# Kernel optimization log

Measured on AMD Instinct MI355X. Metric: run time of the kernel, lower is better.

Reference implementation:

```python
import jax, jax.numpy as jnp
import numpy as np

V, E, H, B, S, O, L = 50257, 256, 512, 64, 1024, 1, 2


def setup_inputs() -> dict:
    key = jax.random.key(0)
    ks = jax.random.split(key, 16)
    s = 0.02
    d = {
        "tokens": jax.random.randint(ks[0], (B, S), 0, V),
        "emb": jax.random.normal(ks[1], (V, E), jnp.float32) * s,
        "fc_w": jax.random.normal(ks[2], (O, H), jnp.float32) * s,
        "fc_b": jnp.zeros((O,), jnp.float32),
    }
    ins = [E, H]
    for l in range(L):
        i = ins[l]
        d[f"gate_w{l}"] = jax.random.normal(ks[3 + 4 * l], (2 * H, i + H), jnp.float32) * s
        d[f"gate_b{l}"] = jnp.zeros((2 * H,), jnp.float32)
        d[f"gi_w{l}"] = jax.random.normal(ks[4 + 4 * l], (H, i), jnp.float32) * s
        d[f"gi_b{l}"] = jnp.zeros((H,), jnp.float32)
        d[f"gh_w{l}"] = jax.random.normal(ks[5 + 4 * l], (H, H), jnp.float32) * s
        d[f"gh_b{l}"] = jnp.zeros((H,), jnp.float32)
    return d


def _cell(x, h, gw, gb, giw, gib, ghw, ghb):
    # gates from concat(input, hidden): [B, 2H]
    gates = jnp.concatenate([x, h], axis=-1) @ gw.T + gb
    r, z = jnp.split(gates, 2, axis=-1)
    r = jax.nn.sigmoid(r)
    z = jax.nn.sigmoid(z)
    n = jnp.tanh(x @ giw.T + gib + r * (h @ ghw.T + ghb))
    return (1.0 - z) * n + z * h  # dropout is identity at inference


def _forward(tokens, emb, fc_w, fc_b, layers):
    x = emb[tokens]  # [B, S, E]
    b = tokens.shape[0]
    h0 = tuple(jnp.zeros((b, H), x.dtype) for _ in layers)

    def step(hs, xt):  # xt: [B, E]
        new = []
        inp = xt
        for h, p in zip(hs, layers):
            h = _cell(inp, h, *p)
            new.append(h)
            inp = h
        return tuple(new), None

    hs, _ = jax.lax.scan(step, h0, jnp.swapaxes(x, 0, 1))  # scan over S
    out = hs[-1] @ fc_w.T + fc_b  # [B, 1]
    return jax.nn.sigmoid(jnp.squeeze(out))  # [B]


def reference(tokens, emb, fc_w, fc_b,
              gate_w0, gate_b0, gi_w0, gi_b0, gh_w0, gh_b0,
              gate_w1, gate_b1, gi_w1, gi_b1, gh_w1, gh_b1):
    layers = [
        (gate_w0, gate_b0, gi_w0, gi_b0, gh_w0, gh_b0),
        (gate_w1, gate_b1, gi_w1, gi_b1, gh_w1, gh_b1),
    ]
    return _forward(tokens, emb, fc_w, fc_b, layers)
```

## Files before the change

### kernel.cpp

```cpp
#include <hip/hip_runtime.h>

typedef _Float16 f16;
typedef _Float16 f16x8 __attribute__((ext_vector_type(8)));
typedef float f32x4 __attribute__((ext_vector_type(4)));
typedef unsigned long long u64;

#define B_ 64
#define S_ 1024
#define E_ 256
#define H_ 512
#define NG 1536
#define TCH 128
#define NCHUNK (S_/TCH)
#define ROWS_CH (TCH*B_)
#define HS_LD 544

__device__ __forceinline__ float sigm(float x) { return 1.f / (1.f + __expf(-x)); }

#define ALOAD(p) __hip_atomic_load((p), __ATOMIC_RELAXED, __HIP_MEMORY_SCOPE_AGENT)
#define ASTORE(p, v) __hip_atomic_store((p), (v), __ATOMIC_RELAXED, __HIP_MEMORY_SCOPE_AGENT)

__global__ __launch_bounds__(256) void k_embed(const int* __restrict__ tok,
        const float* __restrict__ emb, f16* __restrict__ X, int t0) {
    int idx = blockIdx.x * 256 + threadIdx.x;
    int r = idx >> 6;
    int c4 = (idx & 63) << 2;
    int t = t0 + (r >> 6), b = r & 63;
    int tk = tok[b * S_ + t];
    float4 v = *reinterpret_cast<const float4*>(emb + (size_t)tk * E_ + c4);
    union { f16 h[4]; u64 u; } w;
    w.h[0] = (f16)v.x; w.h[1] = (f16)v.y; w.h[2] = (f16)v.z; w.h[3] = (f16)v.w;
    *reinterpret_cast<u64*>(X + (size_t)r * E_ + c4) = w.u;
}

__global__ __launch_bounds__(256) void k_packW(const float* __restrict__ gw, int ld, int off,
        const float* __restrict__ g2, f16* __restrict__ W, int KK) {
    int idx = blockIdx.x * 256 + threadIdx.x;
    int per = KK >> 2;
    if (idx >= NG * per) return;
    int row = idx / per;
    int c4 = (idx % per) << 2;
    const float* src = (row < 1024) ? gw + (size_t)row * ld + off + c4
                                    : g2 + (size_t)(row - 1024) * KK + c4;
    float4 v = *reinterpret_cast<const float4*>(src);
    union { f16 h[4]; u64 u; } w;
    w.h[0] = (f16)v.x; w.h[1] = (f16)v.y; w.h[2] = (f16)v.z; w.h[3] = (f16)v.w;
    *reinterpret_cast<u64*>(W + (size_t)row * KK + c4) = w.u;
}

__global__ __launch_bounds__(256) void k_packBias(const float* __restrict__ gb,
        const float* __restrict__ gib, float* __restrict__ bias) {
    int i = blockIdx.x * 256 + threadIdx.x;
    if (i < 1024) bias[i] = gb[i];
    else if (i < NG) bias[i] = gib[i - 1024];
}

__global__ __launch_bounds__(256) void k_gemm(const f16* __restrict__ A,
        const f16* __restrict__ Bm, const float* __restrict__ bias,
        f16* __restrict__ C, int K) {
    __shared__ f16 As[64][40];
    __shared__ f16 Bs[64][40];
    const int tid = threadIdx.x;
    const int m0 = blockIdx.y << 6, n0 = blockIdx.x << 6;
    const int w = tid >> 6, l = tid & 63;
    const int wr = (w >> 1) << 5, wc = (w & 1) << 5;
    const int srow = tid >> 2, sc8 = (tid & 3) << 3;
    const int fr = l & 15, kl = (l >> 4) << 3;
    f32x4 acc[2][2] = {};
    for (int k0 = 0; k0 < K; k0 += 32) {
        *reinterpret_cast<f16x8*>(&As[srow][sc8]) =
            *reinterpret_cast<const f16x8*>(A + (size_t)(m0 + srow) * K + k0 + sc8);
        *reinterpret_cast<f16x8*>(&Bs[srow][sc8]) =
            *reinterpret_cast<const f16x8*>(Bm + (size_t)(n0 + srow) * K + k0 + sc8);
        __syncthreads();
        f16x8 a0 = *reinterpret_cast<const f16x8*>(&As[wr + fr][kl]);
        f16x8 a1 = *reinterpret_cast<const f16x8*>(&As[wr + 16 + fr][kl]);
        f16x8 b0 = *reinterpret_cast<const f16x8*>(&Bs[wc + fr][kl]);
        f16x8 b1 = *reinterpret_cast<const f16x8*>(&Bs[wc + 16 + fr][kl]);
        acc[0][0] = __builtin_amdgcn_mfma_f32_16x16x32_f16(a0, b0, acc[0][0], 0, 0, 0);
        acc[0][1] = __builtin_amdgcn_mfma_f32_16x16x32_f16(a0, b1, acc[0][1], 0, 0, 0);
        acc[1][0] = __builtin_amdgcn_mfma_f32_16x16x32_f16(a1, b0, acc[1][0], 0, 0, 0);
        acc[1][1] = __builtin_amdgcn_mfma_f32_16x16x32_f16(a1, b1, acc[1][1], 0, 0, 0);
        __syncthreads();
    }
    for (int fm = 0; fm < 2; ++fm)
        for (int fn = 0; fn < 2; ++fn) {
            int col = n0 + wc + (fn << 4) + fr;
            float bv = bias[col];
            for (int j = 0; j < 4; ++j) {
                int rowg = m0 + wr + (fm << 4) + ((l >> 4) << 2) + j;
                C[(size_t)rowg * NG + col] = (f16)(acc[fm][fn][j] + bv);
            }
        }
}

__global__ __launch_bounds__(256, 1) void k_recur4(
        const f16* __restrict__ Wh0p, const f16* __restrict__ Wh1p,
        const f16* __restrict__ Z0, const f16* __restrict__ Z1,
        const float* __restrict__ ghb0, const float* __restrict__ ghb1,
        u64* ring0, u64* ring1, f16* __restrict__ H0out, f16* __restrict__ h1out,
        int t00, int n0, int t01, int n1) {
    __shared__ __align__(16) f16 HS[8][HS_LD];
    __shared__ __align__(16) f16 hx[8][40];
    const int blk = blockIdx.x;
    const int c = blk & 7;
    const int l = (blk >> 3) & 1;
    const int gg = blk >> 4;
    const int nsteps = l ? n1 : n0;
    if (nsteps <= 0) return;
    const int t0 = l ? t01 : t00;
    const f16* __restrict__ Wh = l ? Wh1p : Wh0p;
    const f16* __restrict__ Z  = l ? Z1 : Z0;
    const float* __restrict__ ghb = l ? ghb1 : ghb0;
    u64* ring = l ? ring1 : ring0;

    const int i0 = gg << 5;
    const int tid = threadIdx.x;
    const int w = tid >> 6;
    const int lane = tid & 63;
    const int colb = lane & 15;
    const int bq = lane & 7;
    const int j4 = lane >> 4;
    const int rrow = lane & 15;
    const int ol = rrow >> 2, gate = rrow & 3;

    f16x8 wA[2][16];
    #pragma unroll
    for (int tl = 0; tl < 2; ++tl) {
        const int out = i0 + (w << 3) + (tl << 2) + ol;
        #pragma unroll
        for (int t = 0; t < 16; ++t) {
            f16x8 v{};
            if (gate < 3)
                v = *reinterpret_cast<const f16x8*>(
                        Wh + ((size_t)(gate * H_ + out)) * H_ + (t << 5) + (j4 << 3));
            wA[tl][t] = v;
        }
    }
    const int outA = i0 + (w << 3) + j4;
    const int outB = outA + 4;
    const float gbA = ghb[outA], gbB = ghb[outB];

    for (int sl = 0; sl < nsteps; ++sl) {
        const int s = t0 + sl;
        const size_t zrow = ((size_t)sl * 64 + (c << 3) + bq) * NG;
        float zrA = (float)Z[zrow + outA];
        float zzA = (float)Z[zrow + H_ + outA];
        float znA = (float)Z[zrow + 2 * H_ + outA];
        float zrB = (float)Z[zrow + outB];
        float zzB = (float)Z[zrow + H_ + outB];
        float znB = (float)Z[zrow + 2 * H_ + outB];
        {
            const u64* src = ring + ((size_t)(s & 3) * 8 + c) * 2048;
            u64 g[8];
            #pragma unroll
            for (int i = 0; i < 8; ++i) g[i] = ALOAD(src + (i << 8) + tid);
            #pragma unroll
            for (int i = 0; i < 8; ++i) {
                while ((unsigned)(g[i] >> 32) != (unsigned)s)
                    g[i] = ALOAD(src + (i << 8) + tid);
                *reinterpret_cast<unsigned*>(
                    &HS[i][((tid >> 4) << 5) + ((tid & 15) << 1)]) = (unsigned)g[i];
            }
        }
        __syncthreads();
        f32x4 a00{}, a01{}, a10{}, a11{};
        #pragma unroll
        for (int t = 0; t < 16; ++t) {
            f16x8 bf = *reinterpret_cast<const f16x8*>(&HS[bq][(t << 5) + (j4 << 3)]);
            if (t & 1) {
                a01 = __builtin_amdgcn_mfma_f32_16x16x32_f16(wA[0][t], bf, a01, 0, 0, 0);
                a11 = __builtin_amdgcn_mfma_f32_16x16x32_f16(wA[1][t], bf, a11, 0, 0, 0);
            } else {
                a00 = __builtin_amdgcn_mfma_f32_16x16x32_f16(wA[0][t], bf, a00, 0, 0, 0);
                a10 = __builtin_amdgcn_mfma_f32_16x16x32_f16(wA[1][t], bf, a10, 0, 0, 0);
            }
        }
        f32x4 dA = a00 + a01;
        f32x4 dB = a10 + a11;
        if (colb < 8) {
            float holdA = (float)HS[bq][outA];
            float holdB = (float)HS[bq][outB];
            float rA = sigm(zrA + dA[0]);
            float zA = sigm(zzA + dA[1]);
            float nA = tanhf(znA + rA * (dA[2] + gbA));
            float rB = sigm(zrB + dB[0]);
            float zB = sigm(zzB + dB[1]);
            float nB = tanhf(znB + rB * (dB[2] + gbB));
            hx[bq][(w << 3) + j4]     = (f16)((1.f - zA) * nA + zA * holdA);
            hx[bq][(w << 3) + 4 + j4] = (f16)((1.f - zB) * nB + zB * holdB);
        }
        __syncthreads();
        if (tid < 128) {
            const int b = tid >> 4, d = tid & 15;
            unsigned dval = *reinterpret_cast<const unsigned*>(&hx[b][d << 1]);
            u64 gr = ((u64)(unsigned)(s + 1) << 32) | (u64)dval;
            ASTORE(ring + ((size_t)((s + 1) & 3) * 8 + c) * 2048
                        + ((size_t)b << 8) + (gg << 4) + d, gr);
            if (l == 0)
                *reinterpret_cast<unsigned*>(
                    &H0out[((size_t)sl * 64 + (c << 3) + b) * H_ + i0 + (d << 1)]) = dval;
            else if (s == S_ - 1)
                *reinterpret_cast<unsigned*>(
                    &h1out[((size_t)(c << 3) + b) * H_ + i0 + (d << 1)]) = dval;
        }
        __syncthreads();
    }
}

__global__ __launch_bounds__(64) void k_final(const f16* __restrict__ h,
        const float* __restrict__ fcw, const float* __restrict__ fcb,
        float* __restrict__ out) {
    int b = threadIdx.x;
    float acc = fcb[0];
    for (int k = 0; k < H_; ++k) acc += (float)h[(size_t)b * H_ + k] * fcw[k];
    out[b] = sigm(acc);
}

extern "C" void kernel_launch(void* const* d_in, const int* in_sizes, int n_in,
                              void* d_out, int out_size, void* d_ws, size_t ws_size,
                              hipStream_t stream) {
    (void)in_sizes; (void)n_in; (void)out_size; (void)ws_size;
    const int*   tokens = (const int*)d_in[0];
    const float* emb  = (const float*)d_in[1];
    const float* fc_w = (const float*)d_in[2];
    const float* fc_b = (const float*)d_in[3];
    const float* gw0  = (const float*)d_in[4];
    const float* gb0  = (const float*)d_in[5];
    const float* giw0 = (const float*)d_in[6];
    const float* gib0 = (const float*)d_in[7];
    const float* ghw0 = (const float*)d_in[8];
    const float* ghb0 = (const float*)d_in[9];
    const float* gw1  = (const float*)d_in[10];
    const float* gb1  = (const float*)d_in[11];
    const float* giw1 = (const float*)d_in[12];
    const float* gib1 = (const float*)d_in[13];
    const float* ghw1 = (const float*)d_in[14];
    const float* ghb1 = (const float*)d_in[15];

    char* base = (char*)d_ws;
    size_t off = 0;
    auto carve = [&](size_t bytes) {
        char* p = base + off;
        off = (off + bytes + 255) & ~(size_t)255;
        return p;
    };
    f16*   Wx0   = (f16*)carve((size_t)NG * 256 * 2);
    f16*   Wh0   = (f16*)carve((size_t)NG * 512 * 2);
    f16*   Wx1   = (f16*)carve((size_t)NG * 512 * 2);
    f16*   Wh1   = (f16*)carve((size_t)NG * 512 * 2);
    float* bias0 = (float*)carve(NG * 4);
    float* bias1 = (float*)carve(NG * 4);
    u64*   ring0 = (u64*)carve((size_t)4 * 8 * 2048 * 8);
    u64*   ring1 = (u64*)carve((size_t)4 * 8 * 2048 * 8);
    f16*   h1out = (f16*)carve((size_t)B_ * H_ * 2);
    f16*   Xc    = (f16*)carve((size_t)ROWS_CH * 256 * 2);
    f16*   Zc0   = (f16*)carve((size_t)ROWS_CH * NG * 2);
    f16*   H0c   = (f16*)carve((size_t)ROWS_CH * 512 * 2);
    f16*   Zc1   = (f16*)carve((size_t)ROWS_CH * NG * 2);

    hipMemsetAsync(ring0, 0, (size_t)4 * 8 * 2048 * 8, stream);
    hipMemsetAsync(ring1, 0, (size_t)4 * 8 * 2048 * 8, stream);

    k_packW<<<384, 256, 0, stream>>>(gw0, 768, 0,    giw0, Wx0, 256);
    k_packW<<<768, 256, 0, stream>>>(gw0, 768, 256,  ghw0, Wh0, 512);
    k_packW<<<768, 256, 0, stream>>>(gw1, 1024, 0,   giw1, Wx1, 512);
    k_packW<<<768, 256, 0, stream>>>(gw1, 1024, 512, ghw1, Wh1, 512);
    k_packBias<<<6, 256, 0, stream>>>(gb0, gib0, bias0);
    k_packBias<<<6, 256, 0, stream>>>(gb1, gib1, bias1);

    dim3 gemmGrid(NG / 64, ROWS_CH / 64);
    for (int ch = 0; ch < NCHUNK; ++ch) {
        int t0 = ch * TCH;
        k_embed<<<ROWS_CH * 64 / 256, 256, 0, stream>>>(tokens, emb, Xc, t0);
        k_gemm<<<gemmGrid, 256, 0, stream>>>(Xc, Wx0, bias0, Zc0, 256);
        k_recur4<<<256, 256, 0, stream>>>(Wh0, Wh1, Zc0, Zc1, ghb0, ghb1,
                                          ring0, ring1, H0c, h1out,
                                          t0, TCH, t0 - TCH, ch ? TCH : 0);
        k_gemm<<<gemmGrid, 256, 0, stream>>>(H0c, Wx1, bias1, Zc1, 512);
    }
    k_recur4<<<256, 256, 0, stream>>>(Wh0, Wh1, Zc0, Zc1, ghb0, ghb1,
                                      ring0, ring1, H0c, h1out,
                                      0, 0, (NCHUNK - 1) * TCH, TCH);
    k_final<<<1, 64, 0, stream>>>(h1out, fc_w, fc_b, (float*)d_out);
}
```

Before: 3.143 ms.

## Double-buffer recurrent hidden state, publish directly from lanes, prefetch next Z

After: 5.002 ms. 1.59x slower.

```diff
diff --git a/kernel.cpp b/kernel.cpp
--- a/kernel.cpp
+++ b/kernel.cpp
@@ -94,14 +94,13 @@
         }
 }
 
-__global__ __launch_bounds__(256, 1) void k_recur4(
+__global__ __launch_bounds__(256, 1) void k_recur5(
         const f16* __restrict__ Wh0p, const f16* __restrict__ Wh1p,
         const f16* __restrict__ Z0, const f16* __restrict__ Z1,
         const float* __restrict__ ghb0, const float* __restrict__ ghb1,
         u64* ring0, u64* ring1, f16* __restrict__ H0out, f16* __restrict__ h1out,
         int t00, int n0, int t01, int n1) {
-    __shared__ __align__(16) f16 HS[8][HS_LD];
-    __shared__ __align__(16) f16 hx[8][40];
+    __shared__ __align__(16) f16 HS[2][8][HS_LD];
     const int blk = blockIdx.x;
     const int c = blk & 7;
     const int l = (blk >> 3) & 1;
@@ -141,33 +140,61 @@
     const int outB = outA + 4;
     const float gbA = ghb[outA], gbB = ghb[outB];
 
+    float zrA, zzA, znA, zrB, zzB, znB;
+    {
+        const size_t zrow = ((size_t)(c << 3) + bq) * NG;
+        zrA = (float)Z[zrow + outA]; zzA = (float)Z[zrow + H_ + outA];
+        znA = (float)Z[zrow + 2 * H_ + outA];
+        zrB = (float)Z[zrow + outB]; zzB = (float)Z[zrow + H_ + outB];
+        znB = (float)Z[zrow + 2 * H_ + outB];
+    }
+
     for (int sl = 0; sl < nsteps; ++sl) {
         const int s = t0 + sl;
-        const size_t zrow = ((size_t)sl * 64 + (c << 3) + bq) * NG;
-        float zrA = (float)Z[zrow + outA];
-        float zzA = (float)Z[zrow + H_ + outA];
-        float znA = (float)Z[zrow + 2 * H_ + outA];
-        float zrB = (float)Z[zrow + outB];
-        float zzB = (float)Z[zrow + H_ + outB];
-        float znB = (float)Z[zrow + 2 * H_ + outB];
+        f16* Hc = &HS[sl & 1][0][0];
         {
             const u64* src = ring + ((size_t)(s & 3) * 8 + c) * 2048;
             u64 g[8];
             #pragma unroll
             for (int i = 0; i < 8; ++i) g[i] = ALOAD(src + (i << 8) + tid);
+            unsigned miss = 0;
             #pragma unroll
             for (int i = 0; i < 8; ++i) {
-                while ((unsigned)(g[i] >> 32) != (unsigned)s)
-                    g[i] = ALOAD(src + (i << 8) + tid);
-                *reinterpret_cast<unsigned*>(
-                    &HS[i][((tid >> 4) << 5) + ((tid & 15) << 1)]) = (unsigned)g[i];
+                if ((unsigned)(g[i] >> 32) == (unsigned)s) {
+                    const int rest = tid, b = i;
+                    const int og = ((rest >> 4) << 5) + (((rest >> 2) & 3) << 3) + (rest & 3);
+                    Hc[b * HS_LD + og]     = __builtin_bit_cast(f16, (unsigned short)(g[i] & 0xffff));
+                    Hc[b * HS_LD + og + 4] = __builtin_bit_cast(f16, (unsigned short)((g[i] >> 16) & 0xffff));
+                } else miss |= 1u << i;
+            }
+            while (miss) {
+                #pragma unroll
+                for (int i = 0; i < 8; ++i)
+                    if (miss & (1u << i)) g[i] = ALOAD(src + (i << 8) + tid);
+                #pragma unroll
+                for (int i = 0; i < 8; ++i)
+                    if ((miss & (1u << i)) && (unsigned)(g[i] >> 32) == (unsigned)s) {
+                        const int rest = tid, b = i;
+                        const int og = ((rest >> 4) << 5) + (((rest >> 2) & 3) << 3) + (rest & 3);
+                        Hc[b * HS_LD + og]     = __builtin_bit_cast(f16, (unsigned short)(g[i] & 0xffff));
+                        Hc[b * HS_LD + og + 4] = __builtin_bit_cast(f16, (unsigned short)((g[i] >> 16) & 0xffff));
+                        miss &= ~(1u << i);
+                    }
             }
         }
         __syncthreads();
+        float nrA = 0, nzA = 0, nnA = 0, nrB = 0, nzB = 0, nnB = 0;
+        if (sl + 1 < nsteps) {
+            const size_t zrow = ((size_t)(sl + 1) * 64 + (c << 3) + bq) * NG;
+            nrA = (float)Z[zrow + outA]; nzA = (float)Z[zrow + H_ + outA];
+            nnA = (float)Z[zrow + 2 * H_ + outA];
+            nrB = (float)Z[zrow + outB]; nzB = (float)Z[zrow + H_ + outB];
+            nnB = (float)Z[zrow + 2 * H_ + outB];
+        }
         f32x4 a00{}, a01{}, a10{}, a11{};
         #pragma unroll
         for (int t = 0; t < 16; ++t) {
-            f16x8 bf = *reinterpret_cast<const f16x8*>(&HS[bq][(t << 5) + (j4 << 3)]);
+            f16x8 bf = *reinterpret_cast<const f16x8*>(&Hc[bq * HS_LD + (t << 5) + (j4 << 3)]);
             if (t & 1) {
                 a01 = __builtin_amdgcn_mfma_f32_16x16x32_f16(wA[0][t], bf, a01, 0, 0, 0);
                 a11 = __builtin_amdgcn_mfma_f32_16x16x32_f16(wA[1][t], bf, a11, 0, 0, 0);
@@ -179,32 +206,30 @@
         f32x4 dA = a00 + a01;
         f32x4 dB = a10 + a11;
         if (colb < 8) {
-            float holdA = (float)HS[bq][outA];
-            float holdB = (float)HS[bq][outB];
+            float holdA = (float)Hc[bq * HS_LD + outA];
+            float holdB = (float)Hc[bq * HS_LD + outB];
             float rA = sigm(zrA + dA[0]);
             float zA = sigm(zzA + dA[1]);
             float nA = tanhf(znA + rA * (dA[2] + gbA));
             float rB = sigm(zrB + dB[0]);
             float zB = sigm(zzB + dB[1]);
             float nB = tanhf(znB + rB * (dB[2] + gbB));
-            hx[bq][(w << 3) + j4]     = (f16)((1.f - zA) * nA + zA * holdA);
-            hx[bq][(w << 3) + 4 + j4] = (f16)((1.f - zB) * nB + zB * holdB);
-        }
-        __syncthreads();
-        if (tid < 128) {
-            const int b = tid >> 4, d = tid & 15;
-            unsigned dval = *reinterpret_cast<const unsigned*>(&hx[b][d << 1]);
-            u64 gr = ((u64)(unsigned)(s + 1) << 32) | (u64)dval;
-            ASTORE(ring + ((size_t)((s + 1) & 3) * 8 + c) * 2048
-                        + ((size_t)b << 8) + (gg << 4) + d, gr);
-            if (l == 0)
-                *reinterpret_cast<unsigned*>(
-                    &H0out[((size_t)sl * 64 + (c << 3) + b) * H_ + i0 + (d << 1)]) = dval;
-            else if (s == S_ - 1)
-                *reinterpret_cast<unsigned*>(
-                    &h1out[((size_t)(c << 3) + b) * H_ + i0 + (d << 1)]) = dval;
-        }
-        __syncthreads();
+            f16 hA = (f16)((1.f - zA) * nA + zA * holdA);
+            f16 hB = (f16)((1.f - zB) * nB + zB * holdB);
+            unsigned short uA = __builtin_bit_cast(unsigned short, hA);
+            unsigned short uB = __builtin_bit_cast(unsigned short, hB);
+            u64 gr = ((u64)(unsigned)(s + 1) << 32) | ((u64)uB << 16) | (u64)uA;
+            const size_t gi = ((size_t)bq << 8) + (gg << 4) + (w << 2) + j4;
+            ASTORE(ring + ((size_t)((s + 1) & 3) * 8 + c) * 2048 + gi, gr);
+            if (l == 0) {
+                f16* hp = H0out + ((size_t)sl * 64 + (c << 3) + bq) * H_;
+                hp[outA] = hA; hp[outB] = hB;
+            } else if (s == S_ - 1) {
+                f16* hp = h1out + ((size_t)(c << 3) + bq) * H_;
+                hp[outA] = hA; hp[outB] = hB;
+            }
+        }
+        zrA = nrA; zzA = nzA; znA = nnA; zrB = nrB; zzB = nzB; znB = nnB;
     }
 }
 
@@ -274,12 +299,12 @@
         int t0 = ch * TCH;
         k_embed<<<ROWS_CH * 64 / 256, 256, 0, stream>>>(tokens, emb, Xc, t0);
         k_gemm<<<gemmGrid, 256, 0, stream>>>(Xc, Wx0, bias0, Zc0, 256);
-        k_recur4<<<256, 256, 0, stream>>>(Wh0, Wh1, Zc0, Zc1, ghb0, ghb1,
+        k_recur5<<<256, 256, 0, stream>>>(Wh0, Wh1, Zc0, Zc1, ghb0, ghb1,
                                           ring0, ring1, H0c, h1out,
                                           t0, TCH, t0 - TCH, ch ? TCH : 0);
         k_gemm<<<gemmGrid, 256, 0, stream>>>(H0c, Wx1, bias1, Zc1, 512);
     }
-    k_recur4<<<256, 256, 0, stream>>>(Wh0, Wh1, Zc0, Zc1, ghb0, ghb1,
+    k_recur5<<<256, 256, 0, stream>>>(Wh0, Wh1, Zc0, Zc1, ghb0, ghb1,
                                       ring0, ring1, H0c, h1out,
                                       0, 0, (NCHUNK - 1) * TCH, TCH);
     k_final<<<1, 64, 0, stream>>>(h1out, fc_w, fc_b, (float*)d_out);
```

## Fuse chunked GEMMs and recurrence into one persistent producer-consumer megakernel

Applied to the files above, without the earlier changes.

After: 3.568 ms. 1.14x slower.

```diff
diff --git a/kernel.cpp b/kernel.cpp
--- a/kernel.cpp
+++ b/kernel.cpp
@@ -10,27 +10,25 @@
 #define E_ 256
 #define H_ 512
 #define NG 1536
-#define TCH 128
-#define NCHUNK (S_/TCH)
-#define ROWS_CH (TCH*B_)
+#define V_ 50257
 #define HS_LD 544
+#define ZSLOT 32
+#define DSLOT 64
 
 __device__ __forceinline__ float sigm(float x) { return 1.f / (1.f + __expf(-x)); }
 
 #define ALOAD(p) __hip_atomic_load((p), __ATOMIC_RELAXED, __HIP_MEMORY_SCOPE_AGENT)
 #define ASTORE(p, v) __hip_atomic_store((p), (v), __ATOMIC_RELAXED, __HIP_MEMORY_SCOPE_AGENT)
-
-__global__ __launch_bounds__(256) void k_embed(const int* __restrict__ tok,
-        const float* __restrict__ emb, f16* __restrict__ X, int t0) {
-    int idx = blockIdx.x * 256 + threadIdx.x;
-    int r = idx >> 6;
-    int c4 = (idx & 63) << 2;
-    int t = t0 + (r >> 6), b = r & 63;
-    int tk = tok[b * S_ + t];
-    float4 v = *reinterpret_cast<const float4*>(emb + (size_t)tk * E_ + c4);
-    union { f16 h[4]; u64 u; } w;
-    w.h[0] = (f16)v.x; w.h[1] = (f16)v.y; w.h[2] = (f16)v.z; w.h[3] = (f16)v.w;
-    *reinterpret_cast<u64*>(X + (size_t)r * E_ + c4) = w.u;
+#define AADD(p, v) __hip_atomic_fetch_add((p), (v), __ATOMIC_RELAXED, __HIP_MEMORY_SCOPE_AGENT)
+
+__device__ __forceinline__ float zxt(u64 g, int odd) {
+    unsigned short u = (unsigned short)(odd ? (g >> 16) : g);
+    return (float)__builtin_bit_cast(f16, u);
+}
+__device__ __forceinline__ u64 pk2(float a, float b) {
+    unsigned short ua = __builtin_bit_cast(unsigned short, (f16)a);
+    unsigned short ub = __builtin_bit_cast(unsigned short, (f16)b);
+    return (u64)ua | ((u64)ub << 16);
 }
 
 __global__ __launch_bounds__(256) void k_packW(const float* __restrict__ gw, int ld, int off,
@@ -55,156 +53,279 @@
     else if (i < NG) bias[i] = gib[i - 1024];
 }
 
-__global__ __launch_bounds__(256) void k_gemm(const f16* __restrict__ A,
-        const f16* __restrict__ Bm, const float* __restrict__ bias,
-        f16* __restrict__ C, int K) {
-    __shared__ f16 As[64][40];
-    __shared__ f16 Bs[64][40];
+__global__ __launch_bounds__(256) void k_embconv(const float* __restrict__ emb,
+        f16* __restrict__ out) {
+    long long i = (long long)blockIdx.x * 256 + threadIdx.x;
+    if (i >= (long long)V_ * E_ / 4) return;
+    float4 v = reinterpret_cast<const float4*>(emb)[i];
+    union { f16 h[4]; u64 u; } w;
+    w.h[0] = (f16)v.x; w.h[1] = (f16)v.y; w.h[2] = (f16)v.z; w.h[3] = (f16)v.w;
+    reinterpret_cast<u64*>(out)[i] = w.u;
+}
+
+__global__ __launch_bounds__(256, 2) void k_mega(
+    const f16* __restrict__ Wx0, const f16* __restrict__ Wh0,
+    const f16* __restrict__ Wx1, const f16* __restrict__ Wh1,
+    const float* __restrict__ bias0c, const float* __restrict__ bias1c,
+    const float* __restrict__ ghb0, const float* __restrict__ ghb1,
+    const int* __restrict__ tok, const f16* __restrict__ embh,
+    u64* ring0, u64* ring1, u64* d0r, u64* z0r, u64* z1r,
+    int* zflag1, f16* __restrict__ h1out)
+{
+    __shared__ __align__(16) unsigned char LDS_[65536];
+    const int blk = blockIdx.x;
     const int tid = threadIdx.x;
-    const int m0 = blockIdx.y << 6, n0 = blockIdx.x << 6;
-    const int w = tid >> 6, l = tid & 63;
-    const int wr = (w >> 1) << 5, wc = (w & 1) << 5;
-    const int srow = tid >> 2, sc8 = (tid & 3) << 3;
-    const int fr = l & 15, kl = (l >> 4) << 3;
-    f32x4 acc[2][2] = {};
-    for (int k0 = 0; k0 < K; k0 += 32) {
-        *reinterpret_cast<f16x8*>(&As[srow][sc8]) =
-            *reinterpret_cast<const f16x8*>(A + (size_t)(m0 + srow) * K + k0 + sc8);
-        *reinterpret_cast<f16x8*>(&Bs[srow][sc8]) =
-            *reinterpret_cast<const f16x8*>(Bm + (size_t)(n0 + srow) * K + k0 + sc8);
-        __syncthreads();
-        f16x8 a0 = *reinterpret_cast<const f16x8*>(&As[wr + fr][kl]);
-        f16x8 a1 = *reinterpret_cast<const f16x8*>(&As[wr + 16 + fr][kl]);
-        f16x8 b0 = *reinterpret_cast<const f16x8*>(&Bs[wc + fr][kl]);
-        f16x8 b1 = *reinterpret_cast<const f16x8*>(&Bs[wc + 16 + fr][kl]);
-        acc[0][0] = __builtin_amdgcn_mfma_f32_16x16x32_f16(a0, b0, acc[0][0], 0, 0, 0);
-        acc[0][1] = __builtin_amdgcn_mfma_f32_16x16x32_f16(a0, b1, acc[0][1], 0, 0, 0);
-        acc[1][0] = __builtin_amdgcn_mfma_f32_16x16x32_f16(a1, b0, acc[1][0], 0, 0, 0);
-        acc[1][1] = __builtin_amdgcn_mfma_f32_16x16x32_f16(a1, b1, acc[1][1], 0, 0, 0);
-        __syncthreads();
-    }
-    for (int fm = 0; fm < 2; ++fm)
-        for (int fn = 0; fn < 2; ++fn) {
-            int col = n0 + wc + (fn << 4) + fr;
-            float bv = bias[col];
-            for (int j = 0; j < 4; ++j) {
-                int rowg = m0 + wr + (fm << 4) + ((l >> 4) << 2) + j;
-                C[(size_t)rowg * NG + col] = (f16)(acc[fm][fn][j] + bv);
+
+    if (blk < 256) {
+        const int l = blk >> 7;
+        const int q = blk & 127;
+        const int c = q & 7, gg = q >> 3;
+        const int i0 = gg << 5;
+        const int w = tid >> 6, lane = tid & 63;
+        const int colb = lane & 15, bq = lane & 7, j4 = lane >> 4;
+        const int rrow = lane & 15;
+        const int ol = rrow >> 2, gate = rrow & 3;
+        const f16* Wh = l ? Wh1 : Wh0;
+        const float* ghb = l ? ghb1 : ghb0;
+        u64* ring = l ? ring1 : ring0;
+        const u64* zr = l ? z1r : z0r;
+        f16* HS = (f16*)LDS_;
+        f16* hx = (f16*)(LDS_ + 8 * HS_LD * 2);
+
+        f16x8 wA[2][16];
+        #pragma unroll
+        for (int tl = 0; tl < 2; ++tl) {
+            const int out = i0 + (w << 3) + (tl << 2) + ol;
+            #pragma unroll
+            for (int t = 0; t < 16; ++t) {
+                f16x8 v{};
+                if (gate < 3)
+                    v = *reinterpret_cast<const f16x8*>(
+                            Wh + ((size_t)(gate * H_ + out)) * H_ + (t << 5) + (j4 << 3));
+                wA[tl][t] = v;
             }
         }
-}
-
-__global__ __launch_bounds__(256, 1) void k_recur4(
-        const f16* __restrict__ Wh0p, const f16* __restrict__ Wh1p,
-        const f16* __restrict__ Z0, const f16* __restrict__ Z1,
-        const float* __restrict__ ghb0, const float* __restrict__ ghb1,
-        u64* ring0, u64* ring1, f16* __restrict__ H0out, f16* __restrict__ h1out,
-        int t00, int n0, int t01, int n1) {
-    __shared__ __align__(16) f16 HS[8][HS_LD];
-    __shared__ __align__(16) f16 hx[8][40];
-    const int blk = blockIdx.x;
-    const int c = blk & 7;
-    const int l = (blk >> 3) & 1;
-    const int gg = blk >> 4;
-    const int nsteps = l ? n1 : n0;
-    if (nsteps <= 0) return;
-    const int t0 = l ? t01 : t00;
-    const f16* __restrict__ Wh = l ? Wh1p : Wh0p;
-    const f16* __restrict__ Z  = l ? Z1 : Z0;
-    const float* __restrict__ ghb = l ? ghb1 : ghb0;
-    u64* ring = l ? ring1 : ring0;
-
-    const int i0 = gg << 5;
-    const int tid = threadIdx.x;
-    const int w = tid >> 6;
-    const int lane = tid & 63;
-    const int colb = lane & 15;
-    const int bq = lane & 7;
-    const int j4 = lane >> 4;
-    const int rrow = lane & 15;
-    const int ol = rrow >> 2, gate = rrow & 3;
-
-    f16x8 wA[2][16];
-    #pragma unroll
-    for (int tl = 0; tl < 2; ++tl) {
-        const int out = i0 + (w << 3) + (tl << 2) + ol;
+        const int outA = i0 + (w << 3) + j4, outB = outA + 4;
+        const float gbA = ghb[outA], gbB = ghb[outB];
+        const int batch = (c << 3) + bq;
+        const int par = j4 & 1;
+        const size_t zoA = (size_t)(outA >> 1), zoB = (size_t)(outB >> 1);
+
+        for (int s = 0; s < S_; ++s) {
+            const u64* zs = zr + (size_t)(s & (ZSLOT - 1)) * 49152 + (size_t)batch * 768;
+            u64 zg0 = ALOAD(zs + zoA),        zg1 = ALOAD(zs + zoB);
+            u64 zg2 = ALOAD(zs + 256 + zoA),  zg3 = ALOAD(zs + 256 + zoB);
+            u64 zg4 = ALOAD(zs + 512 + zoA),  zg5 = ALOAD(zs + 512 + zoB);
+            if (!l && s >= 64) {
+                const int* zf = zflag1 + (s - 60);
+                while (ALOAD(zf) < 24) {}
+            }
+            {
+                const u64* src = ring + ((size_t)(s & 3) * 8 + c) * 2048;
+                u64 g[8];
+                #pragma unroll
+                for (int i = 0; i < 8; ++i) g[i] = ALOAD(src + (i << 8) + tid);
+                #pragma unroll
+                for (int i = 0; i < 8; ++i) {
+                    while ((unsigned)(g[i] >> 32) != (unsigned)s)
+                        g[i] = ALOAD(src + (i << 8) + tid);
+                    *reinterpret_cast<unsigned*>(
+                        &HS[i * HS_LD + ((tid >> 4) << 5) + ((tid & 15) << 1)]) = (unsigned)g[i];
+                }
+            }
+            const unsigned ztg = (unsigned)(s + 1);
+            while ((unsigned)(zg0 >> 32) != ztg) zg0 = ALOAD(zs + zoA);
+            while ((unsigned)(zg1 >> 32) != ztg) zg1 = ALOAD(zs + zoB);
+            while ((unsigned)(zg2 >> 32) != ztg) zg2 = ALOAD(zs + 256 + zoA);
+            while ((unsigned)(zg3 >> 32) != ztg) zg3 = ALOAD(zs + 256 + zoB);
+            while ((unsigned)(zg4 >> 32) != ztg) zg4 = ALOAD(zs + 512 + zoA);
+            while ((unsigned)(zg5 >> 32) != ztg) zg5 = ALOAD(zs + 512 + zoB);
+            __syncthreads();
+            f32x4 a00{}, a01{}, a10{}, a11{};
+            #pragma unroll
+            for (int t = 0; t < 16; ++t) {
+                f16x8 bf = *reinterpret_cast<const f16x8*>(&HS[bq * HS_LD + (t << 5) + (j4 << 3)]);
+                if (t & 1) {
+                    a01 = __builtin_amdgcn_mfma_f32_16x16x32_f16(wA[0][t], bf, a01, 0, 0, 0);
+                    a11 = __builtin_amdgcn_mfma_f32_16x16x32_f16(wA[1][t], bf, a11, 0, 0, 0);
+                } else {
+                    a00 = __builtin_amdgcn_mfma_f32_16x16x32_f16(wA[0][t], bf, a00, 0, 0, 0);
+                    a10 = __builtin_amdgcn_mfma_f32_16x16x32_f16(wA[1][t], bf, a10, 0, 0, 0);
+                }
+            }
+            f32x4 dA = a00 + a01, dB = a10 + a11;
+            if (colb < 8) {
+                float holdA = (float)HS[bq * HS_LD + outA];
+                float holdB = (float)HS[bq * HS_LD + outB];
+                float rA = sigm(zxt(zg0, par) + dA[0]);
+                float zA = sigm(zxt(zg2, par) + dA[1]);
+                float nA = tanhf(zxt(zg4, par) + rA * (dA[2] + gbA));
+                float rB = sigm(zxt(zg1, par) + dB[0]);
+                float zB = sigm(zxt(zg3, par) + dB[1]);
+                float nB = tanhf(zxt(zg5, par) + rB * (dB[2] + gbB));
+                hx[bq * 40 + (w << 3) + j4]     = (f16)((1.f - zA) * nA + zA * holdA);
+                hx[bq * 40 + (w << 3) + 4 + j4] = (f16)((1.f - zB) * nB + zB * holdB);
+            }
+            __syncthreads();
+            if (tid < 128) {
+                const int b = tid >> 4, d = tid & 15;
+                unsigned dval = *reinterpret_cast<const unsigned*>(&hx[b * 40 + (d << 1)]);
+                u64 gr = ((u64)(unsigned)(s + 1) << 32) | (u64)dval;
+                const size_t gi = ((size_t)b << 8) + (gg << 4) + d;
+                ASTORE(ring + ((size_t)((s + 1) & 3) * 8 + c) * 2048 + gi, gr);
+                if (!l)
+                    ASTORE(d0r + ((size_t)((s + 1) & (DSLOT - 1)) * 8 + c) * 2048 + gi, gr);
+                else if (s == S_ - 1)
+                    *reinterpret_cast<unsigned*>(
+                        &h1out[((size_t)(c << 3) + b) * H_ + i0 + (d << 1)]) = dval;
+            }
+            __syncthreads();
+        }
+    } else if (blk < 352) {
+        const int qq = blk - 256, p = qq & 3, nt = qq >> 2;
+        const int n0 = nt << 6;
+        const int w = tid >> 6, lane = tid & 63;
+        const int q4 = lane >> 4, l15 = lane & 15;
+        f16* hst = (f16*)LDS_;
+        f16x8 wxa[16];
+        const int arow = n0 + (w << 4) + l15;
         #pragma unroll
-        for (int t = 0; t < 16; ++t) {
-            f16x8 v{};
-            if (gate < 3)
-                v = *reinterpret_cast<const f16x8*>(
-                        Wh + ((size_t)(gate * H_ + out)) * H_ + (t << 5) + (j4 << 3));
-            wA[tl][t] = v;
+        for (int t = 0; t < 16; ++t)
+            wxa[t] = *reinterpret_cast<const f16x8*>(Wx1 + (size_t)arow * 512 + (t << 5) + (q4 << 3));
+        const int cb = n0 + (w << 4) + (q4 << 2);
+        const float bv0 = bias1c[cb], bv1 = bias1c[cb + 1], bv2 = bias1c[cb + 2], bv3 = bias1c[cb + 3];
+        const int sx = (l15 & 7) << 3;
+
+        for (int t = p; t < S_; t += 4) {
+            if (t >= 32) {
+                const u64* pr = ring1 + ((size_t)((t - 28) & 3) * 8 + (lane & 7)) * 2048;
+                while (!__all((int)(unsigned)(ALOAD(pr) >> 32) >= t - 28)) {}
+            }
+            {
+                const u64* src = d0r + (size_t)((t + 1) & (DSLOT - 1)) * 16384;
+                const unsigned tg = (unsigned)(t + 1);
+                #pragma unroll
+                for (int hf = 0; hf < 4; ++hf) {
+                    u64 g[16]; unsigned miss = 0;
+                    #pragma unroll
+                    for (int j = 0; j < 16; ++j) g[j] = ALOAD(src + (hf << 12) + (j << 8) + tid);
+                    #pragma unroll
+                    for (int j = 0; j < 16; ++j) {
+                        int idx = (hf << 12) + (j << 8) + tid;
+                        int bt = idx >> 8, col = (idx & 255) << 1;
+                        if ((unsigned)(g[j] >> 32) == tg)
+                            *reinterpret_cast<unsigned*>(&hst[bt * 512 + (col ^ ((bt & 7) << 3))]) = (unsigned)g[j];
+                        else miss |= 1u << j;
+                    }
+                    while (miss) {
+                        #pragma unroll
+                        for (int j = 0; j < 16; ++j) if (miss & (1u << j)) {
+                            u64 v = ALOAD(src + (hf << 12) + (j << 8) + tid);
+                            if ((unsigned)(v >> 32) == tg) {
+                                int idx = (hf << 12) + (j << 8) + tid;
+                                int bt = idx >> 8, col = (idx & 255) << 1;
+                                *reinterpret_cast<unsigned*>(&hst[bt * 512 + (col ^ ((bt & 7) << 3))]) = (unsigned)v;
+                                miss &= ~(1u << j);
+                            }
+                        }
+                    }
+                }
+            }
+            __syncthreads();
+            if (tid == 0) AADD(zflag1 + t, 1);
+            f32x4 ac0{}, ac1{}, ac2{}, ac3{};
+            #pragma unroll
+            for (int t16 = 0; t16 < 16; ++t16) {
+                const int ko = ((t16 << 5) + (q4 << 3)) ^ sx;
+                f16x8 b0 = *reinterpret_cast<const f16x8*>(&hst[(l15)      * 512 + ko]);
+                f16x8 b1 = *reinterpret_cast<const f16x8*>(&hst[(16 + l15) * 512 + ko]);
+                f16x8 b2 = *reinterpret_cast<const f16x8*>(&hst[(32 + l15) * 512 + ko]);
+                f16x8 b3 = *reinterpret_cast<const f16x8*>(&hst[(48 + l15) * 512 + ko]);
+                ac0 = __builtin_amdgcn_mfma_f32_16x16x32_f16(wxa[t16], b0, ac0, 0, 0, 0);
+                ac1 = __builtin_amdgcn_mfma_f32_16x16x32_f16(wxa[t16], b1, ac1, 0, 0, 0);
+                ac2 = __builtin_amdgcn_mfma_f32_16x16x32_f16(wxa[t16], b2, ac2, 0, 0, 0);
+                ac3 = __builtin_amdgcn_mfma_f32_16x16x32_f16(wxa[t16], b3, ac3, 0, 0, 0);
+            }
+            {
+                const u64 t64 = (u64)(unsigned)(t + 1) << 32;
+                u64* zb = z1r + (size_t)(t & (ZSLOT - 1)) * 49152 + (cb >> 1);
+                u64* b0 = zb + (size_t)(l15) * 768;
+                ASTORE(b0,     t64 | pk2(ac0[0] + bv0, ac0[1] + bv1));
+                ASTORE(b0 + 1, t64 | pk2(ac0[2] + bv2, ac0[3] + bv3));
+                u64* b1 = zb + (size_t)(16 + l15) * 768;
+                ASTORE(b1,     t64 | pk2(ac1[0] + bv0, ac1[1] + bv1));
+                ASTORE(b1 + 1, t64 | pk2(ac1[2] + bv2, ac1[3] + bv3));
+                u64* b2 = zb + (size_t)(32 + l15) * 768;
+                ASTORE(b2,     t64 | pk2(ac2[0] + bv0, ac2[1] + bv1));
+                ASTORE(b2 + 1, t64 | pk2(ac2[2] + bv2, ac2[3] + bv3));
+                u64* b3 = zb + (size_t)(48 + l15) * 768;
+                ASTORE(b3,     t64 | pk2(ac3[0] + bv0, ac3[1] + bv1));
+                ASTORE(b3 + 1, t64 | pk2(ac3[2] + bv2, ac3[3] + bv3));
+            }
+            __syncthreads();
         }
-    }
-    const int outA = i0 + (w << 3) + j4;
-    const int outB = outA + 4;
-    const float gbA = ghb[outA], gbB = ghb[outB];
-
-    for (int sl = 0; sl < nsteps; ++sl) {
-        const int s = t0 + sl;
-        const size_t zrow = ((size_t)sl * 64 + (c << 3) + bq) * NG;
-        float zrA = (float)Z[zrow + outA];
-        float zzA = (float)Z[zrow + H_ + outA];
-        float znA = (float)Z[zrow + 2 * H_ + outA];
-        float zrB = (float)Z[zrow + outB];
-        float zzB = (float)Z[zrow + H_ + outB];
-        float znB = (float)Z[zrow + 2 * H_ + outB];
-        {
-            const u64* src = ring + ((size_t)(s & 3) * 8 + c) * 2048;
-            u64 g[8];
+    } else {
+        const int qq = blk - 352, p = qq & 1, nt = qq >> 1;
+        const int n0 = nt << 6;
+        const int w = tid >> 6, lane = tid & 63;
+        const int q4 = lane >> 4, l15 = lane & 15;
+        f16* xst = (f16*)LDS_;
+        f16x8 wxa[8];
+        const int arow = n0 + (w << 4) + l15;
+        #pragma unroll
+        for (int t = 0; t < 8; ++t)
+            wxa[t] = *reinterpret_cast<const f16x8*>(Wx0 + (size_t)arow * 256 + (t << 5) + (q4 << 3));
+        const int cb = n0 + (w << 4) + (q4 << 2);
+        const float bv0 = bias0c[cb], bv1 = bias0c[cb + 1], bv2 = bias0c[cb + 2], bv3 = bias0c[cb + 3];
+        const int sx = (l15 & 7) << 3;
+        const int sb = tid >> 2, seg = tid & 3;
+        const int ssx = (sb & 7) << 3;
+
+        for (int t = p; t < S_; t += 2) {
+            if (t >= 32) {
+                const u64* pr = ring0 + ((size_t)((t - 28) & 3) * 8 + (lane & 7)) * 2048;
+                while (!__all((int)(unsigned)(ALOAD(pr) >> 32) >= t - 28)) {}
+            }
+            {
+                int tk = tok[sb * S_ + t];
+                const f16* ep = embh + (size_t)tk * E_ + (seg << 6);
+                #pragma unroll
+                for (int j = 0; j < 8; ++j)
+                    *reinterpret_cast<f16x8*>(&xst[sb * 256 + ((((seg << 6) + (j << 3))) ^ ssx)]) =
+                        *reinterpret_cast<const f16x8*>(ep + (j << 3));
+            }
+            __syncthreads();
+            f32x4 ac0{}, ac1{}, ac2{}, ac3{};
             #pragma unroll
-            for (int i = 0; i < 8; ++i) g[i] = ALOAD(src + (i << 8) + tid);
-            #pragma unroll
-            for (int i = 0; i < 8; ++i) {
-                while ((unsigned)(g[i] >> 32) != (unsigned)s)
-                    g[i] = ALOAD(src + (i << 8) + tid);
-                *reinterpret_cast<unsigned*>(
-                    &HS[i][((tid >> 4) << 5) + ((tid & 15) << 1)]) = (unsigned)g[i];
-            }
+            for (int t8 = 0; t8 < 8; ++t8) {
+                const int ko = ((t8 << 5) + (q4 << 3)) ^ sx;
+                f16x8 b0 = *reinterpret_cast<const f16x8*>(&xst[(l15)      * 256 + ko]);
+                f16x8 b1 = *reinterpret_cast<const f16x8*>(&xst[(16 + l15) * 256 + ko]);
+                f16x8 b2 = *reinterpret_cast<const f16x8*>(&xst[(32 + l15) * 256 + ko]);
+                f16x8 b3 = *reinterpret_cast<const f16x8*>(&xst[(48 + l15) * 256 + ko]);
+                ac0 = __builtin_amdgcn_mfma_f32_16x16x32_f16(wxa[t8], b0, ac0, 0, 0, 0);
+                ac1 = __builtin_amdgcn_mfma_f32_16x16x32_f16(wxa[t8], b1, ac1, 0, 0, 0);
+                ac2 = __builtin_amdgcn_mfma_f32_16x16x32_f16(wxa[t8], b2, ac2, 0, 0, 0);
+                ac3 = __builtin_amdgcn_mfma_f32_16x16x32_f16(wxa[t8], b3, ac3, 0, 0, 0);
+            }
+            {
+                const u64 t64 = (u64)(unsigned)(t + 1) << 32;
+                u64* zb = z0r + (size_t)(t & (ZSLOT - 1)) * 49152 + (cb >> 1);
+                u64* b0 = zb + (size_t)(l15) * 768;
+                ASTORE(b0,     t64 | pk2(ac0[0] + bv0, ac0[1] + bv1));
+                ASTORE(b0 + 1, t64 | pk2(ac0[2] + bv2, ac0[3] + bv3));
+                u64* b1 = zb + (size_t)(16 + l15) * 768;
+                ASTORE(b1,     t64 | pk2(ac1[0] + bv0, ac1[1] + bv1));
+                ASTORE(b1 + 1, t64 | pk2(ac1[2] + bv2, ac1[3] + bv3));
+                u64* b2 = zb + (size_t)(32 + l15) * 768;
+                ASTORE(b2,     t64 | pk2(ac2[0] + bv0, ac2[1] + bv1));
+                ASTORE(b2 + 1, t64 | pk2(ac2[2] + bv2, ac2[3] + bv3));
+                u64* b3 = zb + (size_t)(48 + l15) * 768;
+                ASTORE(b3,     t64 | pk2(ac3[0] + bv0, ac3[1] + bv1));
+                ASTORE(b3 + 1, t64 | pk2(ac3[2] + bv2, ac3[3] + bv3));
+            }
+            __syncthreads();
         }
-        __syncthreads();
-        f32x4 a00{}, a01{}, a10{}, a11{};
-        #pragma unroll
-        for (int t = 0; t < 16; ++t) {
-            f16x8 bf = *reinterpret_cast<const f16x8*>(&HS[bq][(t << 5) + (j4 << 3)]);
-            if (t & 1) {
-                a01 = __builtin_amdgcn_mfma_f32_16x16x32_f16(wA[0][t], bf, a01, 0, 0, 0);
-                a11 = __builtin_amdgcn_mfma_f32_16x16x32_f16(wA[1][t], bf, a11, 0, 0, 0);
-            } else {
-                a00 = __builtin_amdgcn_mfma_f32_16x16x32_f16(wA[0][t], bf, a00, 0, 0, 0);
-                a10 = __builtin_amdgcn_mfma_f32_16x16x32_f16(wA[1][t], bf, a10, 0, 0, 0);
-            }
-        }
-        f32x4 dA = a00 + a01;
-        f32x4 dB = a10 + a11;
-        if (colb < 8) {
-            float holdA = (float)HS[bq][outA];
-            float holdB = (float)HS[bq][outB];
-            float rA = sigm(zrA + dA[0]);
-            float zA = sigm(zzA + dA[1]);
-            float nA = tanhf(znA + rA * (dA[2] + gbA));
-            float rB = sigm(zrB + dB[0]);
-            float zB = sigm(zzB + dB[1]);
-            float nB = tanhf(znB + rB * (dB[2] + gbB));
-            hx[bq][(w << 3) + j4]     = (f16)((1.f - zA) * nA + zA * holdA);
-            hx[bq][(w << 3) + 4 + j4] = (f16)((1.f - zB) * nB + zB * holdB);
-        }
-        __syncthreads();
-        if (tid < 128) {
-            const int b = tid >> 4, d = tid & 15;
-            unsigned dval = *reinterpret_cast<const unsigned*>(&hx[b][d << 1]);
-            u64 gr = ((u64)(unsigned)(s + 1) << 32) | (u64)dval;
-            ASTORE(ring + ((size_t)((s + 1) & 3) * 8 + c) * 2048
-                        + ((size_t)b << 8) + (gg << 4) + d, gr);
-            if (l == 0)
-                *reinterpret_cast<unsigned*>(
-                    &H0out[((size_t)sl * 64 + (c << 3) + b) * H_ + i0 + (d << 1)]) = dval;
-            else if (s == S_ - 1)
-                *reinterpret_cast<unsigned*>(
-                    &h1out[((size_t)(c << 3) + b) * H_ + i0 + (d << 1)]) = dval;
-        }
-        __syncthreads();
     }
 }
 
@@ -245,42 +366,36 @@
         off = (off + bytes + 255) & ~(size_t)255;
         return p;
     };
-    f16*   Wx0   = (f16*)carve((size_t)NG * 256 * 2);
-    f16*   Wh0   = (f16*)carve((size_t)NG * 512 * 2);
-    f16*   Wx1   = (f16*)carve((size_t)NG * 512 * 2);
-    f16*   Wh1   = (f16*)carve((size_t)NG * 512 * 2);
-    float* bias0 = (float*)carve(NG * 4);
-    float* bias1 = (float*)carve(NG * 4);
-    u64*   ring0 = (u64*)carve((size_t)4 * 8 * 2048 * 8);
-    u64*   ring1 = (u64*)carve((size_t)4 * 8 * 2048 * 8);
-    f16*   h1out = (f16*)carve((size_t)B_ * H_ * 2);
-    f16*   Xc    = (f16*)carve((size_t)ROWS_CH * 256 * 2);
-    f16*   Zc0   = (f16*)carve((size_t)ROWS_CH * NG * 2);
-    f16*   H0c   = (f16*)carve((size_t)ROWS_CH * 512 * 2);
-    f16*   Zc1   = (f16*)carve((size_t)ROWS_CH * NG * 2);
+    f16*   embh   = (f16*)carve((size_t)V_ * E_ * 2);
+    f16*   Wx0    = (f16*)carve((size_t)NG * 256 * 2);
+    f16*   Wh0    = (f16*)carve((size_t)NG * 512 * 2);
+    f16*   Wx1    = (f16*)carve((size_t)NG * 512 * 2);
+    f16*   Wh1    = (f16*)carve((size_t)NG * 512 * 2);
+    float* bias0c = (float*)carve(NG * 4);
+    float* bias1c = (float*)carve(NG * 4);
+    u64*   ring0  = (u64*)carve((size_t)4 * 8 * 2048 * 8);
+    u64*   ring1  = (u64*)carve((size_t)4 * 8 * 2048 * 8);
+    u64*   d0r    = (u64*)carve((size_t)DSLOT * 8 * 2048 * 8);
+    u64*   z0r    = (u64*)carve((size_t)ZSLOT * 49152 * 8);
+    u64*   z1r    = (u64*)carve((size_t)ZSLOT * 49152 * 8);
+    int*   zflag1 = (int*)carve((size_t)S_ * 4);
+    f16*   h1out  = (f16*)carve((size_t)B_ * H_ * 2);
 
     hipMemsetAsync(ring0, 0, (size_t)4 * 8 * 2048 * 8, stream);
     hipMemsetAsync(ring1, 0, (size_t)4 * 8 * 2048 * 8, stream);
-
+    hipMemsetAsync(d0r, 0, (size_t)DSLOT * 8 * 2048 * 8, stream);
+    hipMemsetAsync(zflag1, 0, (size_t)S_ * 4, stream);
+
+    k_embconv<<<(V_ * E_ / 4 + 255) / 256, 256, 0, stream>>>(emb, embh);
     k_packW<<<384, 256, 0, stream>>>(gw0, 768, 0,    giw0, Wx0, 256);
     k_packW<<<768, 256, 0, stream>>>(gw0, 768, 256,  ghw0, Wh0, 512);
     k_packW<<<768, 256, 0, stream>>>(gw1, 1024, 0,   giw1, Wx1, 512);
     k_packW<<<768, 256, 0, stream>>>(gw1, 1024, 512, ghw1, Wh1, 512);
-    k_packBias<<<6, 256, 0, stream>>>(gb0, gib0, bias0);
-    k_packBias<<<6, 256, 0, stream>>>(gb1, gib1, bias1);
-
-    dim3 gemmGrid(NG / 64, ROWS_CH / 64);
-    for (int ch = 0; ch < NCHUNK; ++ch) {
-        int t0 = ch * TCH;
-        k_embed<<<ROWS_CH * 64 / 256, 256, 0, stream>>>(tokens, emb, Xc, t0);
-        k_gemm<<<gemmGrid, 256, 0, stream>>>(Xc, Wx0, bias0, Zc0, 256);
-        k_recur4<<<256, 256, 0, stream>>>(Wh0, Wh1, Zc0, Zc1, ghb0, ghb1,
-                                          ring0, ring1, H0c, h1out,
-                                          t0, TCH, t0 - TCH, ch ? TCH : 0);
-        k_gemm<<<gemmGrid, 256, 0, stream>>>(H0c, Wx1, bias1, Zc1, 512);
-    }
-    k_recur4<<<256, 256, 0, stream>>>(Wh0, Wh1, Zc0, Zc1, ghb0, ghb1,
-                                      ring0, ring1, H0c, h1out,
-                                      0, 0, (NCHUNK - 1) * TCH, TCH);
+    k_packBias<<<6, 256, 0, stream>>>(gb0, gib0, bias0c);
+    k_packBias<<<6, 256, 0, stream>>>(gb1, gib1, bias1c);
+
+    k_mega<<<400, 256, 0, stream>>>(Wx0, Wh0, Wx1, Wh1, bias0c, bias1c,
+                                    ghb0, ghb1, tokens, embh,
+                                    ring0, ring1, d0r, z0r, z1r, zflag1, h1out);
     k_final<<<1, 64, 0, stream>>>(h1out, fc_w, fc_b, (float*)d_out);
 }
```
